# Performance work log

Hardware: AMD Instinct MI355X
Metric: run time of the kernel (lower is better)

The kernel has to match this reference:

```python
import jax, jax.numpy as jnp
import numpy as np

N_FREQ = 50  # n_frequencies in Model.__init__


def _sine_tables(n_freq):
    i = np.arange(1, n_freq + 1, dtype=np.float32)
    base = 1.0 / (1000.0 ** (2.0 * i / n_freq))           # [n_freq]
    freqs = np.repeat(base, 2)                             # [2*n_freq]
    shifts = np.tile(np.array([0.0, np.pi / 2], dtype=np.float32), n_freq)  # [2*n_freq]
    return jnp.asarray(freqs), jnp.asarray(shifts)


def setup_inputs() -> dict:
    key = jax.random.key(0)
    ks = jax.random.split(key, 8)
    n_frag, n_genes, d_sine, d_emb = 200000, 500, 4 * N_FREQ, 10
    cell_n, gene_n = 200, 500
    coordinates = jax.random.normal(ks[0], (n_frag, 2), dtype=jnp.float32) * 1000.0
    stdv = 1.0 / np.sqrt(d_emb)
    w1 = jax.random.uniform(ks[1], (n_genes, d_sine, d_emb), jnp.float32, -stdv, stdv)
    b1 = jnp.zeros((n_genes, d_emb), jnp.float32)
    w2 = jnp.ones((n_genes, d_emb), jnp.float32)
    b2 = jnp.zeros((n_genes,), jnp.float32)
    genemapping = jax.random.randint(ks[2], (n_frag,), 0, n_genes, dtype=jnp.int64 if jax.config.jax_enable_x64 else jnp.int32)
    local_cellxgene_ix = jax.random.randint(ks[3], (n_frag,), 0, cell_n * gene_n, dtype=genemapping.dtype)
    genes_oi = jnp.arange(gene_n, dtype=genemapping.dtype)
    return {
        "coordinates": coordinates, "w1": w1, "b1": b1, "w2": w2, "b2": b2,
        "genemapping": genemapping, "local_cellxgene_ix": local_cellxgene_ix,
        "genes_oi": genes_oi, "cell_n": cell_n, "gene_n": gene_n,
    }


def reference(coordinates, w1, b1, w2, b2, genemapping, local_cellxgene_ix, genes_oi, cell_n, gene_n):
    freqs, shifts = _sine_tables(N_FREQ)
    n_frag = coordinates.shape[0]
    # SineEncoding: [n_frag, 2, 2*n_freq] -> [n_frag, 4*n_freq]
    emb = jnp.sin(coordinates[..., None] * freqs + shifts).reshape(n_frag, -1)
    # FragmentEmbedder: per-fragment gene-specific linear + sigmoid
    h = jnp.einsum('fs,fsd->fd', emb, w1[genemapping]) + b1[genemapping]
    h = jax.nn.sigmoid(h)
    # EmbeddingGenePooler: scatter-sum into cell x gene bins
    pooled = jax.ops.segment_sum(h, local_cellxgene_ix, num_segments=cell_n * gene_n)
    cge = pooled.reshape(cell_n, gene_n, -1)
    # EmbeddingToExpression: gene-specific dot + bias
    out = (cge * w2[genes_oi]).sum(-1) + b2[genes_oi]
    return out
```

## Files before the change

kernel.cpp:

```cpp
#include <hip/hip_runtime.h>
#include <hip/hip_bf16.h>
#include <math.h>

#define NF    50
#define DEMB  10
#define W1G   (4 * NF * DEMB)
#define MAXG  512

#define HTPB   256
#define HCHUNK 4096
#define HFPT   (HCHUNK / HTPB)

typedef __attribute__((ext_vector_type(8))) short short8v;
typedef __attribute__((ext_vector_type(4))) float f32x4v;

__device__ __forceinline__ short f2bf(float f) {
    unsigned u = __float_as_uint(f);
    u += 0x7fffu + ((u >> 16) & 1u);
    return (short)(u >> 16);
}

__global__ __launch_bounds__(HTPB) void hist_init_k(
    const int* __restrict__ gm, int n_frag, int n_genes,
    int* __restrict__ counts_mat,
    float* __restrict__ out, const float* __restrict__ b2,
    const int* __restrict__ genes_oi, int gene_n, int total)
{
    __shared__ int lcnt[MAXG];
    for (int t = threadIdx.x; t < MAXG; t += HTPB) lcnt[t] = 0;
    __syncthreads();

    int base = blockIdx.x * HCHUNK;
#pragma unroll
    for (int j = 0; j < HFPT; ++j) {
        int f = base + j * HTPB + (int)threadIdx.x;
        if (f < n_frag) atomicAdd(&lcnt[gm[f]], 1);
    }

    int nthreads = gridDim.x * HTPB;
    for (int i = blockIdx.x * HTPB + (int)threadIdx.x; i < total; i += nthreads) {
        int col = (int)((unsigned)i % (unsigned)gene_n);
        out[i] = b2[genes_oi[col]];
    }

    __syncthreads();
    int* row = counts_mat + (size_t)blockIdx.x * MAXG;
    for (int t = threadIdx.x; t < MAXG; t += HTPB) row[t] = lcnt[t];
}

__global__ void scan_k(const int* __restrict__ counts_mat, int nblk,
                       int* __restrict__ po, int* __restrict__ cursor,
                       int* __restrict__ cnt, int* __restrict__ w2g,
                       int n_genes, int wmax)
{
    __shared__ int buf[MAXG];
    int tid = threadIdx.x;
    int s = 0;
#pragma unroll 8
    for (int b = 0; b < nblk; ++b) s += counts_mat[(size_t)b * MAXG + tid];
    int pc = ((s + 63) >> 6) << 6;
    buf[tid] = pc;
    __syncthreads();
    for (int d = 1; d < MAXG; d <<= 1) {
        int t = (tid >= d) ? buf[tid - d] : 0;
        __syncthreads();
        buf[tid] += t;
        __syncthreads();
    }
    int incl = buf[tid];
    if (tid < n_genes) {
        po[tid + 1] = incl;
        cursor[tid] = incl - pc;
        cnt[tid]    = s;
        int wbeg = (incl - pc) >> 6;
        int wend = incl >> 6;
        for (int w = wbeg; w < wend; ++w) w2g[w] = tid;
    }
    if (tid == 0) po[0] = 0;
    __syncthreads();
    int W = buf[n_genes - 1] >> 6;
    for (int w = W + tid; w < wmax; w += MAXG) w2g[w] = -1;
}

__global__ __launch_bounds__(HTPB) void scatter_k(
    const int* __restrict__ gm, const float* __restrict__ coords,
    const int* __restrict__ lcg, int* __restrict__ cursor,
    float* __restrict__ xs, int* __restrict__ bins,
    int n_frag, int n_genes)
{
    __shared__ int lcnt[MAXG];
    __shared__ int lbase[MAXG];
    for (int t = threadIdx.x; t < MAXG; t += HTPB) lcnt[t] = 0;
    __syncthreads();

    int base = blockIdx.x * HCHUNK;
    int g[HFPT], lr[HFPT];
#pragma unroll
    for (int j = 0; j < HFPT; ++j) {
        int f = base + j * HTPB + (int)threadIdx.x;
        if (f < n_frag) {
            g[j]  = gm[f];
            lr[j] = atomicAdd(&lcnt[g[j]], 1);
        } else {
            g[j] = -1;
        }
    }
    __syncthreads();
    for (int t = threadIdx.x; t < MAXG; t += HTPB) {
        int c = lcnt[t];
        lbase[t] = c ? atomicAdd(&cursor[t], c) : 0;
    }
    __syncthreads();
#pragma unroll
    for (int j = 0; j < HFPT; ++j) {
        if (g[j] >= 0) {
            int f = base + j * HTPB + (int)threadIdx.x;
            int pos = lbase[g[j]] + lr[j];
            float2 xy = ((const float2*)coords)[f];
            xs[2 * pos + 0] = xy.x;
            xs[2 * pos + 1] = xy.y;
            bins[pos] = lcg[f];
        }
    }
}

__global__ __launch_bounds__(256) void main_mfma_k(
    const float* __restrict__ w1, const float* __restrict__ b1,
    const float* __restrict__ w2, const int* __restrict__ genes_oi,
    const float* __restrict__ xs, const int* __restrict__ bins,
    const int* __restrict__ po, const int* __restrict__ cnt,
    const int* __restrict__ w2g, float* __restrict__ out,
    int gene_n, int wmax)
{
    __shared__ float fr[NF];
    if (threadIdx.x < NF) {
        float ex = (-2.0f * (float)(threadIdx.x + 1) / (float)NF) * 9.965784284662087f;
        fr[threadIdx.x] = exp2f(ex) * 0.15915494309189535f;
    }
    __syncthreads();

    int wid  = threadIdx.x >> 6;
    int lane = threadIdx.x & 63;
    int fw   = blockIdx.x * 4 + wid;

    int g = (fw < wmax) ? w2g[fw] : -1;
    g = __builtin_amdgcn_readfirstlane(g);
    if (g < 0) return;

    int d  = lane & 15;
    int q  = lane >> 4;
    int dc = (d < 10) ? d : 9;

    int start = po[g];
    int count = cnt[g];
    int pos   = fw * 64 + lane;
    bool valid = (pos - start) < count;
    float2 xy = valid ? ((const float2*)xs)[pos] : make_float2(0.0f, 0.0f);

    const float* wg = w1 + (size_t)g * W1G;
    short8v breg[7];
#pragma unroll
    for (int kk = 0; kk < 7; ++kk) {
#pragma unroll
        for (int j = 0; j < 8; ++j) {
            int k  = kk * 32 + q * 8 + j;
            int kc = (k < 200) ? k : 199;
            float v = wg[kc * 10 + dc];
            v = (k < 200 && d < 10) ? v : 0.0f;
            breg[kk][j] = f2bf(v);
        }
    }

    float b1v = b1[(size_t)g * DEMB + dc];
    f32x4v acc[4];
#pragma unroll
    for (int m = 0; m < 4; ++m) { acc[m][0] = b1v; acc[m][1] = b1v; acc[m][2] = b1v; acc[m][3] = b1v; }

#pragma unroll
    for (int m = 0; m < 4; ++m) {
        int srcA = m * 16 + d;
        float ax = __shfl(xy.x, srcA);
        float ay = __shfl(xy.y, srcA);
#pragma unroll
        for (int kk = 0; kk < 7; ++kk) {
            short8v afrag;
#pragma unroll
            for (int jj = 0; jj < 4; ++jj) {
                int k0 = kk * 32 + q * 8 + 2 * jj;
                int cc = (k0 >= 100) ? 1 : 0;
                int ii = (k0 - cc * 100) >> 1;
                ii = (k0 < 200) ? ii : 0;
                float fv = fr[ii];
                float xv = cc ? ay : ax;
                float r = xv * fv; r -= rintf(r);
                afrag[2 * jj]     = f2bf(__builtin_amdgcn_sinf(r));
                afrag[2 * jj + 1] = f2bf(__builtin_amdgcn_cosf(r));
            }
            acc[m] = __builtin_amdgcn_mfma_f32_16x16x32_bf16(afrag, breg[kk], acc[m], 0, 0, 0);
        }
    }

    int bin_own  = valid ? bins[pos] : 0;
    int col_own  = (int)((unsigned)bin_own % (unsigned)gene_n);
    int gidx_own = valid ? genes_oi[col_own] : 0;
    int vown     = valid ? 1 : 0;

#pragma unroll
    for (int m = 0; m < 4; ++m) {
#pragma unroll
        for (int reg = 0; reg < 4; ++reg) {
            int src = m * 16 + q * 4 + reg;
            int b   = __shfl(bin_own, src);
            int gi  = __shfl(gidx_own, src);
            int vf  = __shfl(vown, src);
            float hv = acc[m][reg];
            float w2v = w2[gi * DEMB + dc];
            float sg  = 1.0f / (1.0f + __expf(-hv));
            float s   = (d < 10) ? sg * w2v : 0.0f;
#pragma unroll
            for (int off = 1; off < 16; off <<= 1) s += __shfl_xor(s, off);
            if (d == 0 && vf) atomicAdd(&out[b], s);
        }
    }
}

__global__ __launch_bounds__(256) void frag_naive_k(
    const float* __restrict__ coords, const float* __restrict__ w1,
    const float* __restrict__ b1, const float* __restrict__ w2,
    const int* __restrict__ gm, const int* __restrict__ lcg,
    const int* __restrict__ genes_oi, float* __restrict__ out,
    int gene_n, int n_frag)
{
    __shared__ float fr[NF];
    if (threadIdx.x < NF) {
        float ex = (-2.0f * (float)(threadIdx.x + 1) / (float)NF) * 9.965784284662087f;
        fr[threadIdx.x] = exp2f(ex) * 0.15915494309189535f;
    }
    __syncthreads();

    int f = blockIdx.x * blockDim.x + threadIdx.x;
    if (f >= n_frag) return;
    int g = gm[f];
    const float* wrow  = w1 + (size_t)g * W1G;
    const float* b1row = b1 + (size_t)g * DEMB;
    float x0 = coords[2 * f + 0];
    float x1 = coords[2 * f + 1];

    float h[DEMB];
#pragma unroll
    for (int d = 0; d < DEMB; ++d) h[d] = b1row[d];
#pragma unroll 2
    for (int i = 0; i < NF; ++i) {
        float fv = fr[i];
        float r0 = x0 * fv; r0 -= rintf(r0);
        float r1 = x1 * fv; r1 -= rintf(r1);
        float s0 = __builtin_amdgcn_sinf(r0), c0 = __builtin_amdgcn_cosf(r0);
        float s1 = __builtin_amdgcn_sinf(r1), c1 = __builtin_amdgcn_cosf(r1);
        const float* wa = wrow + (2 * i) * DEMB;
        const float* wb = wrow + (2 * NF + 2 * i) * DEMB;
#pragma unroll
        for (int d = 0; d < DEMB; ++d) {
            h[d] += s0 * wa[d] + c0 * wa[DEMB + d] + s1 * wb[d] + c1 * wb[DEMB + d];
        }
    }
    int bin = lcg[f];
    int col = (int)((unsigned)bin % (unsigned)gene_n);
    const float* w2row = w2 + (size_t)genes_oi[col] * DEMB;
    float sum = 0.0f;
#pragma unroll
    for (int d = 0; d < DEMB; ++d) {
        float sg = 1.0f / (1.0f + __expf(-h[d]));
        sum += sg * w2row[d];
    }
    atomicAdd(&out[bin], sum);
}

__global__ void init_out_k(float* __restrict__ out, const float* __restrict__ b2,
                           const int* __restrict__ genes_oi, int gene_n, int total)
{
    int i = blockIdx.x * blockDim.x + threadIdx.x;
    if (i < total) {
        int col = (int)((unsigned)i % (unsigned)gene_n);
        out[i] = b2[genes_oi[col]];
    }
}

extern "C" void kernel_launch(void* const* d_in, const int* in_sizes, int n_in,
                              void* d_out, int out_size, void* d_ws, size_t ws_size,
                              hipStream_t stream)
{
    const float* coords   = (const float*)d_in[0];
    const float* w1       = (const float*)d_in[1];
    const float* b1       = (const float*)d_in[2];
    const float* w2       = (const float*)d_in[3];
    const float* b2       = (const float*)d_in[4];
    const int*   gm       = (const int*)d_in[5];
    const int*   lcg      = (const int*)d_in[6];
    const int*   genes_oi = (const int*)d_in[7];

    int n_frag  = in_sizes[5];
    int n_genes = in_sizes[4];
    int gene_n  = in_sizes[7];
    int total   = out_size;
    float* out  = (float*)d_out;

    int nblk = (n_frag + HCHUNK - 1) / HCHUNK;
    int wmax = (n_frag >> 6) + n_genes + 1;
    size_t padcap = (size_t)n_frag + 64 * (size_t)n_genes + 64;

    int* counts_mat = (int*)d_ws;
    int* po         = counts_mat + (size_t)nblk * MAXG;
    int* cursor     = po + (MAXG + 1);
    int* cnt        = cursor + MAXG;
    int* w2g        = cnt + MAXG;
    float* xs       = (float*)(w2g + wmax);
    int* bins       = (int*)(xs + 2 * padcap);
    size_t need = ((size_t)nblk * MAXG + (MAXG + 1) + 2 * MAXG + wmax
                   + 3 * padcap) * sizeof(int);

    bool use_sorted = (ws_size >= need) && (n_genes <= MAXG);
    if (use_sorted) {
        hist_init_k<<<nblk, HTPB, 0, stream>>>(gm, n_frag, n_genes, counts_mat,
                                               out, b2, genes_oi, gene_n, total);
        scan_k<<<1, MAXG, 0, stream>>>(counts_mat, nblk, po, cursor, cnt, w2g,
                                       n_genes, wmax);
        scatter_k<<<nblk, HTPB, 0, stream>>>(gm, coords, lcg, cursor,
                                             xs, bins, n_frag, n_genes);
        int mblk = (wmax + 3) / 4;
        main_mfma_k<<<mblk, 256, 0, stream>>>(w1, b1, w2, genes_oi, xs, bins,
                                              po, cnt, w2g, out, gene_n, wmax);
    } else {
        init_out_k<<<(total + 255) / 256, 256, 0, stream>>>(out, b2, genes_oi, gene_n, total);
        frag_naive_k<<<(n_frag + 255) / 256, 256, 0, stream>>>(coords, w1, b1, w2, gm, lcg,
                                                               genes_oi, out, gene_n, n_frag);
    }
}
```

Before: 51.67 us.

## Stage W1 and epilogue through LDS, cache gene W2 per block

W1 rows for each wave's gene are now read with coalesced float4 loads. They are transposed into a per-wave LDS arena as bf16 and then read back as contiguous 16-byte B fragments, replacing the strided scalar gathers. The epilogue writes the MFMA accumulators to LDS so that each lane handles one whole fragment, does the 10-term sigmoid·w2 dot itself, and issues one atomic. This removes the per-row shuffle reductions and broadcasts. W2 rows for genes_oi are preloaded into shared memory per block, which adds a redundant global read per block and about 52KB of LDS that may reduce occupancy.

```diff
diff --git a/kernel.cpp b/kernel.cpp
--- a/kernel.cpp
+++ b/kernel.cpp
@@ -10,6 +10,11 @@
 #define HTPB   256
 #define HCHUNK 4096
 #define HFPT   (HCHUNK / HTPB)
+
+#define KPAD  232
+#define HPAD  19
+#define W2PAD 11
+#define ARENA 7680
 
 typedef __attribute__((ext_vector_type(8))) short short8v;
 typedef __attribute__((ext_vector_type(4))) float f32x4v;
@@ -133,9 +138,18 @@
     int gene_n, int wmax)
 {
     __shared__ float fr[NF];
+    __shared__ float w2l[MAXG * W2PAD];
+    __shared__ __align__(16) char arena[4][ARENA];
+
     if (threadIdx.x < NF) {
         float ex = (-2.0f * (float)(threadIdx.x + 1) / (float)NF) * 9.965784284662087f;
         fr[threadIdx.x] = exp2f(ex) * 0.15915494309189535f;
+    }
+    for (int c = threadIdx.x; c < gene_n; c += 256) {
+        int gi = genes_oi[c];
+#pragma unroll
+        for (int dd = 0; dd < DEMB; ++dd)
+            w2l[c * W2PAD + dd] = w2[(size_t)gi * DEMB + dd];
     }
     __syncthreads();
 
@@ -156,19 +170,36 @@
     int pos   = fw * 64 + lane;
     bool valid = (pos - start) < count;
     float2 xy = valid ? ((const float2*)xs)[pos] : make_float2(0.0f, 0.0f);
-
+    int bin_own = valid ? bins[pos] : 0;
+    int col_own = (int)((unsigned)bin_own % (unsigned)gene_n);
+
+    short* Bw = (short*)(arena[wid]);
     const float* wg = w1 + (size_t)g * W1G;
+#pragma unroll
+    for (int r = 0; r < 8; ++r) {
+        int e4 = r * 64 + lane;
+        if (e4 < W1G / 4) {
+            float4 v = ((const float4*)wg)[e4];
+            int e = e4 * 4;
+            int k0 = e / 10, d0 = e - k0 * 10;
+#pragma unroll
+            for (int c = 0; c < 4; ++c) {
+                Bw[d0 * KPAD + k0] = f2bf((&v.x)[c]);
+                d0++; if (d0 == 10) { d0 = 0; k0++; }
+            }
+        }
+    }
+    for (int idx = lane; idx < 320; idx += 64) {
+        int row = idx >> 5, kz = 200 + (idx & 31);
+        Bw[row * KPAD + kz] = 0;
+    }
+
     short8v breg[7];
-#pragma unroll
-    for (int kk = 0; kk < 7; ++kk) {
-#pragma unroll
-        for (int j = 0; j < 8; ++j) {
-            int k  = kk * 32 + q * 8 + j;
-            int kc = (k < 200) ? k : 199;
-            float v = wg[kc * 10 + dc];
-            v = (k < 200 && d < 10) ? v : 0.0f;
-            breg[kk][j] = f2bf(v);
-        }
+    {
+        const char* bp = arena[wid] + dc * (KPAD * 2) + q * 16;
+#pragma unroll
+        for (int kk = 0; kk < 7; ++kk)
+            breg[kk] = *(const short8v*)(bp + kk * 64);
     }
 
     float b1v = b1[(size_t)g * DEMB + dc];
@@ -200,28 +231,22 @@
         }
     }
 
-    int bin_own  = valid ? bins[pos] : 0;
-    int col_own  = (int)((unsigned)bin_own % (unsigned)gene_n);
-    int gidx_own = valid ? genes_oi[col_own] : 0;
-    int vown     = valid ? 1 : 0;
-
-#pragma unroll
-    for (int m = 0; m < 4; ++m) {
-#pragma unroll
-        for (int reg = 0; reg < 4; ++reg) {
-            int src = m * 16 + q * 4 + reg;
-            int b   = __shfl(bin_own, src);
-            int gi  = __shfl(gidx_own, src);
-            int vf  = __shfl(vown, src);
-            float hv = acc[m][reg];
-            float w2v = w2[gi * DEMB + dc];
-            float sg  = 1.0f / (1.0f + __expf(-hv));
-            float s   = (d < 10) ? sg * w2v : 0.0f;
-#pragma unroll
-            for (int off = 1; off < 16; off <<= 1) s += __shfl_xor(s, off);
-            if (d == 0 && vf) atomicAdd(&out[b], s);
-        }
-    }
+    float* hb = (float*)(arena[wid]);
+#pragma unroll
+    for (int m = 0; m < 4; ++m)
+#pragma unroll
+        for (int r = 0; r < 4; ++r)
+            hb[(m * 16 + q * 4 + r) * HPAD + d] = acc[m][r];
+
+    float sum = 0.0f;
+    const float* wrow2 = &w2l[col_own * W2PAD];
+#pragma unroll
+    for (int dd = 0; dd < DEMB; ++dd) {
+        float hv = hb[lane * HPAD + dd];
+        float sg = 1.0f / (1.0f + __expf(-hv));
+        sum += sg * wrow2[dd];
+    }
+    if (valid) atomicAdd(&out[bin_own], sum);
 }
 
 __global__ __launch_bounds__(256) void frag_naive_k(
```

Measured after the change: 49.89 us. -3.5%, faster.
